# Kernel optimization log

Hardware: AMD Instinct MI355X
Metric: run time of the kernel (lower is better)

## Reference

```python
import jax, jax.numpy as jnp
import numpy as np

EMBED = 1024
HEADS = 16
HEAD_DIM = EMBED // HEADS


def setup_inputs() -> dict:
    key = jax.random.key(0)
    k_x, k_q, k_k, k_v, k_o, k_b = jax.random.split(key, 6)
    s = 1.0 / np.sqrt(EMBED)
    return {
        "x": jax.random.normal(k_x, (4, 2048, EMBED), dtype=jnp.float32),
        "Wq": jax.random.uniform(k_q, (EMBED, EMBED), jnp.float32, -s, s),
        "Wk": jax.random.uniform(k_k, (EMBED, EMBED), jnp.float32, -s, s),
        "Wv": jax.random.uniform(k_v, (EMBED, EMBED), jnp.float32, -s, s),
        "Wo": jax.random.uniform(k_o, (EMBED, EMBED), jnp.float32, -s, s),
        "bo": jax.random.uniform(k_b, (EMBED,), jnp.float32, -s, s),
    }


def reference(x, Wq, Wk, Wv, Wo, bo):
    B, S, E = x.shape
    H, D = HEADS, HEAD_DIM
    # torch nn.Linear: y = x @ W.T
    q = (x @ Wq.T).reshape(B, S, H, D).transpose(0, 2, 1, 3)  # [B,H,S,D]
    k = (x @ Wk.T).reshape(B, S, H, D).transpose(0, 2, 1, 3)
    v = (x @ Wv.T).reshape(B, S, H, D).transpose(0, 2, 1, 3)
    # NOTE: module scales by sqrt(embed_size), not sqrt(head_dim)
    scores = jnp.einsum("bhqd,bhkd->bhqk", q, k) / jnp.sqrt(jnp.float32(E))
    causal = jnp.triu(jnp.ones((S, S), dtype=bool), k=1)
    scores = jnp.where(causal, -jnp.inf, scores)
    attn = jax.nn.softmax(scores, axis=-1)
    out = jnp.einsum("bhqk,bhkd->bhqd", attn, v)  # [B,H,S,D]
    out = out.transpose(0, 2, 1, 3).reshape(B, S, E)
    return out @ Wo.T + bo
```

## Files before the change

kernel.cpp:

```cpp
#include <hip/hip_runtime.h>


#define E_DIM 1024
#define S_LEN 2048
#define BATCH 4
#define NHEAD 16
#define HDIM  64

using short8 = __attribute__((ext_vector_type(8))) short;
using f32x4  = __attribute__((ext_vector_type(4))) float;
using f32x16 = __attribute__((ext_vector_type(16))) float;
using i32x4  = __attribute__((ext_vector_type(4))) int;
using u32x2  = __attribute__((ext_vector_type(2))) unsigned int;

#define GLD16(gp, lp) __builtin_amdgcn_global_load_lds( \
    (const __attribute__((address_space(1))) void*)(gp), \
    (__attribute__((address_space(3))) void*)(lp), 16, 0, 0)

__device__ inline unsigned short f2bf(float f) {
    unsigned int u = __builtin_bit_cast(unsigned int, f);
    u += 0x7FFFu + ((u >> 16) & 1u);
    return (unsigned short)(u >> 16);
}

__device__ inline unsigned int cvt_pk_bf16(float a, float b) {
    unsigned int r;
    asm("v_cvt_pk_bf16_f32 %0, %1, %2" : "=v"(r) : "v"(a), "v"(b));
    return r;
}

__global__ __launch_bounds__(256) void cvt_all(
        const float* __restrict__ x,  const float* __restrict__ wq,
        const float* __restrict__ wk, const float* __restrict__ wv,
        const float* __restrict__ wo,
        unsigned short* __restrict__ xb, unsigned short* __restrict__ wb) {
    const int bid = blockIdx.x;
    const float* src;
    unsigned short* dst;
    int blk;
    if (bid < 8192) { src = x; dst = xb; blk = bid; }
    else {
        const int wsel = (bid - 8192) >> 10;
        blk = (bid - 8192) & 1023;
        src = (wsel == 0) ? wq : (wsel == 1) ? wk : (wsel == 2) ? wv : wo;
        dst = wb + (size_t)wsel * 1048576;
    }
    const int i = (blk * 256 + threadIdx.x) * 4;
    float4 v = *reinterpret_cast<const float4*>(src + i);
    ushort4 o;
    o.x = f2bf(v.x); o.y = f2bf(v.y); o.z = f2bf(v.z); o.w = f2bf(v.w);
    *reinterpret_cast<ushort4*>(dst + i) = o;
}

__global__ __launch_bounds__(256) void gemm_qkv(
        const unsigned short* __restrict__ xb,
        const unsigned short* __restrict__ wb,
        unsigned short* __restrict__ qkv) {
    const int z = blockIdx.z;
    const unsigned short* Bw = wb + (size_t)z * (E_DIM * E_DIM);
    unsigned short* Out = qkv + (size_t)z * ((size_t)BATCH * NHEAD * S_LEN * HDIM);
    const int m0 = blockIdx.x * 128, n0 = blockIdx.y * 128;
    const int tid = threadIdx.x;
    const int lane = tid & 63, w = tid >> 6;
    const int wm = w >> 1, wn = w & 1;
    const int col = lane & 15, hi = lane >> 4;

    __shared__ __align__(16) unsigned short Alds[128 * 32];
    __shared__ __align__(16) unsigned short Blds[128 * 32];

    const int srow = tid >> 2;
    const int sc8  = (tid & 3) * 8;
    const int wofs = w * 512;

    f32x4 acc[4][4] = {};

    for (int kt = 0; kt < E_DIM / 32; ++kt) {
        const int k0 = kt * 32;
        GLD16(xb + (size_t)(m0 + srow) * E_DIM + k0 + sc8,       &Alds[wofs]);
        GLD16(xb + (size_t)(m0 + 64 + srow) * E_DIM + k0 + sc8,  &Alds[2048 + wofs]);
        GLD16(Bw + (size_t)(n0 + srow) * E_DIM + k0 + sc8,       &Blds[wofs]);
        GLD16(Bw + (size_t)(n0 + 64 + srow) * E_DIM + k0 + sc8,  &Blds[2048 + wofs]);
        __syncthreads();
        short8 af[4], bf[4];
#pragma unroll
        for (int mt = 0; mt < 4; ++mt)
            af[mt] = *reinterpret_cast<const short8*>(&Alds[(wm * 64 + mt * 16 + col) * 32 + hi * 8]);
#pragma unroll
        for (int nt = 0; nt < 4; ++nt)
            bf[nt] = *reinterpret_cast<const short8*>(&Blds[(wn * 64 + nt * 16 + col) * 32 + hi * 8]);
#pragma unroll
        for (int mt = 0; mt < 4; ++mt)
#pragma unroll
            for (int nt = 0; nt < 4; ++nt)
                acc[mt][nt] = __builtin_amdgcn_mfma_f32_16x16x32_bf16(af[mt], bf[nt], acc[mt][nt], 0, 0, 0);
        __syncthreads();
    }

    const float scale = (z == 0) ? (0.03125f * 1.44269504f) : 1.0f;
#pragma unroll
    for (int mt = 0; mt < 4; ++mt) {
#pragma unroll
        for (int nt = 0; nt < 4; ++nt) {
#pragma unroll
            for (int b = 0; b < 4; ++b) {
                int m = m0 + wm * 64 + mt * 16 + hi * 4 + b;
                int n = n0 + wn * 64 + nt * 16 + col;
                int bidx = m >> 11, s = m & 2047;
                int h = n >> 6, d = n & 63;
                size_t off = (((size_t)(bidx * NHEAD + h)) * S_LEN + s) * HDIM + d;
                Out[off] = f2bf(acc[mt][nt][b] * scale);
            }
        }
    }
}

__global__ __launch_bounds__(512, 2) void attn_fwd(
        const unsigned short* __restrict__ Q,
        const unsigned short* __restrict__ K,
        const unsigned short* __restrict__ V,
        unsigned short* __restrict__ Out) {
    const int g = blockIdx.x;
    const int qt = 7 - (g >> 6);
    const int bh = (g & 7) + ((g >> 3) & 7) * 8;
    const int b_idx = bh >> 4, h = bh & 15;
    const int tid = threadIdx.x, lane = tid & 63, w = tid >> 6;
    const int l31 = lane & 31, b5 = lane >> 5;
    const int rsw = (l31 & 7) << 3;

    const unsigned short* Qb = Q + (size_t)bh * (S_LEN * HDIM);
    const unsigned short* Kb = K + (size_t)bh * (S_LEN * HDIM);
    const unsigned short* Vb = V + (size_t)bh * (S_LEN * HDIM);

    __shared__ __align__(16) unsigned short Klds[256 * 64];
    __shared__ __align__(16) unsigned short Vt[64 * 256];

    const int krl  = lane >> 3;
    const int kcsw = ((lane & 7) * 8) ^ (krl << 3);
    const int vr = tid & 63, vc8 = (tid >> 6) * 8;

    const int nt = qt + 1;
    const int q0w = qt * 256 + w * 32;
    const int qg = q0w + l31;

    short8 qf[4];
    {
        const unsigned short* qrow = Qb + (size_t)qg * HDIM;
#pragma unroll
        for (int dc = 0; dc < 4; ++dc)
            qf[dc] = *reinterpret_cast<const short8*>(qrow + dc * 16 + b5 * 8);
    }

    f32x16 ot0 = {}, ot1 = {};
    float mrun = -INFINITY, lsum = 0.f;

    short8 pv0 = *reinterpret_cast<const short8*>(Vb + (size_t)(vr) * HDIM + vc8);
    short8 pv1 = *reinterpret_cast<const short8*>(Vb + (size_t)(64 + vr) * HDIM + vc8);
    short8 pv2 = *reinterpret_cast<const short8*>(Vb + (size_t)(128 + vr) * HDIM + vc8);
    short8 pv3 = *reinterpret_cast<const short8*>(Vb + (size_t)(192 + vr) * HDIM + vc8);

    for (int t = 0; t < nt; ++t) {
        const int kv0 = t * 256;
        __syncthreads();
#pragma unroll
        for (int i = 0; i < 4; ++i) {
            const int rowbase = 8 * (8 * i + w);
            GLD16(Kb + (size_t)(kv0 + rowbase + krl) * HDIM + kcsw,
                  &Klds[rowbase * 64]);
        }
#pragma unroll
        for (int j = 0; j < 8; ++j) {
            const int d0 = vc8 + j;
            const int sj = (d0 & 7) << 3;
            Vt[d0 * 256 + ((vr)       ^ sj)] = (unsigned short)pv0[j];
            Vt[d0 * 256 + ((64 + vr)  ^ sj)] = (unsigned short)pv1[j];
            Vt[d0 * 256 + ((128 + vr) ^ sj)] = (unsigned short)pv2[j];
            Vt[d0 * 256 + ((192 + vr) ^ sj)] = (unsigned short)pv3[j];
        }
        if (t < nt - 1) {
            const int kn = kv0 + 256;
            pv0 = *reinterpret_cast<const short8*>(Vb + (size_t)(kn + vr) * HDIM + vc8);
            pv1 = *reinterpret_cast<const short8*>(Vb + (size_t)(kn + 64 + vr) * HDIM + vc8);
            pv2 = *reinterpret_cast<const short8*>(Vb + (size_t)(kn + 128 + vr) * HDIM + vc8);
            pv3 = *reinterpret_cast<const short8*>(Vb + (size_t)(kn + 192 + vr) * HDIM + vc8);
        }
        __syncthreads();

#pragma unroll
        for (int s4 = 0; s4 < 4; ++s4) {
            const int kvs = kv0 + 64 * s4;
            if (kvs > q0w + 31) break;
            const int ksb = 64 * s4;

            f32x16 st0 = {}, st1 = {};
            __builtin_amdgcn_s_setprio(1);
#pragma unroll
            for (int dc = 0; dc < 4; ++dc) {
                const int co = dc * 16 + b5 * 8;
                short8 kfA = *reinterpret_cast<const short8*>(&Klds[(ksb + l31) * 64 + (co ^ rsw)]);
                short8 kfB = *reinterpret_cast<const short8*>(&Klds[(ksb + 32 + l31) * 64 + (co ^ rsw)]);
                st0 = __builtin_amdgcn_mfma_f32_32x32x16_bf16(kfA, qf[dc], st0, 0, 0, 0);
                st1 = __builtin_amdgcn_mfma_f32_32x32x16_bf16(kfB, qf[dc], st1, 0, 0, 0);
            }
            __builtin_amdgcn_s_setprio(0);

            if (kvs + 63 > q0w) {
#pragma unroll
                for (int r = 0; r < 16; ++r) {
                    const int krow = (r & 3) + 8 * (r >> 2) + 4 * b5;
                    if (kvs + krow > qg)      st0[r] = -INFINITY;
                    if (kvs + 32 + krow > qg) st1[r] = -INFINITY;
                }
            }

            float tm0 = fmaxf(st0[0], st1[0]), tm1 = fmaxf(st0[1], st1[1]);
            float tm2 = fmaxf(st0[2], st1[2]), tm3 = fmaxf(st0[3], st1[3]);
            float tm4 = fmaxf(st0[4], st1[4]), tm5 = fmaxf(st0[5], st1[5]);
            float tm6 = fmaxf(st0[6], st1[6]), tm7 = fmaxf(st0[7], st1[7]);
            tm0 = fmaxf(tm0, fmaxf(st0[8],  st1[8]));
            tm1 = fmaxf(tm1, fmaxf(st0[9],  st1[9]));
            tm2 = fmaxf(tm2, fmaxf(st0[10], st1[10]));
            tm3 = fmaxf(tm3, fmaxf(st0[11], st1[11]));
            tm4 = fmaxf(tm4, fmaxf(st0[12], st1[12]));
            tm5 = fmaxf(tm5, fmaxf(st0[13], st1[13]));
            tm6 = fmaxf(tm6, fmaxf(st0[14], st1[14]));
            tm7 = fmaxf(tm7, fmaxf(st0[15], st1[15]));
            tm0 = fmaxf(tm0, tm4); tm1 = fmaxf(tm1, tm5);
            tm2 = fmaxf(tm2, tm6); tm3 = fmaxf(tm3, tm7);
            float vm = fmaxf(fmaxf(tm0, tm1), fmaxf(tm2, tm3));
            vm = fmaxf(vm, __shfl_xor(vm, 32));
            if (__any(vm > mrun + 11.5f)) {
                const float mnew = fmaxf(mrun, vm);
                const float fac = exp2f(mrun - mnew);
                mrun = mnew;
                lsum *= fac;
#pragma unroll
                for (int r = 0; r < 16; ++r) { ot0[r] *= fac; ot1[r] *= fac; }
            }

#pragma unroll
            for (int kc = 0; kc < 4; ++kc) {
                const int r0 = (kc & 1) * 8;
                float pe[8];
#pragma unroll
                for (int i = 0; i < 8; ++i) {
                    const float sv = (kc < 2) ? st0[r0 + i] : st1[r0 + i];
                    pe[i] = exp2f(sv - mrun);
                }
                const float ps = ((pe[0] + pe[1]) + (pe[2] + pe[3]))
                               + ((pe[4] + pe[5]) + (pe[6] + pe[7]));
                lsum += ps;
                const unsigned int W0 = cvt_pk_bf16(pe[0], pe[1]);
                const unsigned int W1 = cvt_pk_bf16(pe[2], pe[3]);
                const unsigned int W2 = cvt_pk_bf16(pe[4], pe[5]);
                const unsigned int W3 = cvt_pk_bf16(pe[6], pe[7]);
                u32x2 s02 = __builtin_amdgcn_permlane32_swap(W0, W2, false, false);
                u32x2 s13 = __builtin_amdgcn_permlane32_swap(W1, W3, false, false);
                i32x4 wv;
                wv[0] = (int)s02[0];
                wv[1] = (int)s13[0];
                wv[2] = (int)s02[1];
                wv[3] = (int)s13[1];
                const short8 pf = __builtin_bit_cast(short8, wv);

                const int ck = ksb + kc * 16 + b5 * 8;
                short8 vf0 = *reinterpret_cast<const short8*>(&Vt[l31 * 256 + (ck ^ rsw)]);
                short8 vf1 = *reinterpret_cast<const short8*>(&Vt[(32 + l31) * 256 + (ck ^ rsw)]);
                __builtin_amdgcn_s_setprio(1);
                ot0 = __builtin_amdgcn_mfma_f32_32x32x16_bf16(vf0, pf, ot0, 0, 0, 0);
                ot1 = __builtin_amdgcn_mfma_f32_32x32x16_bf16(vf1, pf, ot1, 0, 0, 0);
                __builtin_amdgcn_s_setprio(0);
            }
        }
    }

    const float lfull = lsum + __shfl_xor(lsum, 32);
    const float inv = 1.0f / lfull;
    const size_t base = ((size_t)(b_idx * S_LEN + qg)) * E_DIM + h * HDIM;
#pragma unroll
    for (int r2 = 0; r2 < 8; ++r2) {
        const int d0 = 2 * (r2 & 1) + 8 * (r2 >> 1) + 4 * b5;
        const unsigned int u0 = cvt_pk_bf16(ot0[2 * r2] * inv, ot0[2 * r2 + 1] * inv);
        const unsigned int u1 = cvt_pk_bf16(ot1[2 * r2] * inv, ot1[2 * r2 + 1] * inv);
        *reinterpret_cast<unsigned int*>(const_cast<unsigned short*>(Out) + base + d0) = u0;
        *reinterpret_cast<unsigned int*>(const_cast<unsigned short*>(Out) + base + 32 + d0) = u1;
    }
}

__global__ __launch_bounds__(256) void gemm_out(
        const unsigned short* __restrict__ Ab,
        const unsigned short* __restrict__ Bw,
        const float* __restrict__ bias,
        float* __restrict__ Out) {
    const int m0 = blockIdx.x * 128, n0 = blockIdx.y * 128;
    const int tid = threadIdx.x;
    const int lane = tid & 63, w = tid >> 6;
    const int wm = w >> 1, wn = w & 1;
    const int col = lane & 15, hi = lane >> 4;

    __shared__ __align__(16) unsigned short Alds[128 * 32];
    __shared__ __align__(16) unsigned short Blds[128 * 32];

    const int srow = tid >> 2;
    const int sc8  = (tid & 3) * 8;
    const int wofs = w * 512;

    f32x4 acc[4][4] = {};

    for (int kt = 0; kt < E_DIM / 32; ++kt) {
        const int k0 = kt * 32;
        GLD16(Ab + (size_t)(m0 + srow) * E_DIM + k0 + sc8,       &Alds[wofs]);
        GLD16(Ab + (size_t)(m0 + 64 + srow) * E_DIM + k0 + sc8,  &Alds[2048 + wofs]);
        GLD16(Bw + (size_t)(n0 + srow) * E_DIM + k0 + sc8,       &Blds[wofs]);
        GLD16(Bw + (size_t)(n0 + 64 + srow) * E_DIM + k0 + sc8,  &Blds[2048 + wofs]);
        __syncthreads();
        short8 af[4], bf[4];
#pragma unroll
        for (int mt = 0; mt < 4; ++mt)
            af[mt] = *reinterpret_cast<const short8*>(&Alds[(wm * 64 + mt * 16 + col) * 32 + hi * 8]);
#pragma unroll
        for (int nt = 0; nt < 4; ++nt)
            bf[nt] = *reinterpret_cast<const short8*>(&Blds[(wn * 64 + nt * 16 + col) * 32 + hi * 8]);
#pragma unroll
        for (int mt = 0; mt < 4; ++mt)
#pragma unroll
            for (int nt = 0; nt < 4; ++nt)
                acc[mt][nt] = __builtin_amdgcn_mfma_f32_16x16x32_bf16(af[mt], bf[nt], acc[mt][nt], 0, 0, 0);
        __syncthreads();
    }

#pragma unroll
    for (int mt = 0; mt < 4; ++mt) {
#pragma unroll
        for (int nt = 0; nt < 4; ++nt) {
#pragma unroll
            for (int b = 0; b < 4; ++b) {
                int m = m0 + wm * 64 + mt * 16 + hi * 4 + b;
                int n = n0 + wn * 64 + nt * 16 + col;
                Out[(size_t)m * E_DIM + n] = acc[mt][nt][b] + bias[n];
            }
        }
    }
}

extern "C" void kernel_launch(void* const* d_in, const int* in_sizes, int n_in,
                              void* d_out, int out_size, void* d_ws, size_t ws_size,
                              hipStream_t stream) {
    const float* x  = (const float*)d_in[0];
    const float* Wq = (const float*)d_in[1];
    const float* Wk = (const float*)d_in[2];
    const float* Wv = (const float*)d_in[3];
    const float* Wo = (const float*)d_in[4];
    const float* bo = (const float*)d_in[5];
    float* out = (float*)d_out;

    unsigned short* ws   = (unsigned short*)d_ws;
    unsigned short* xb   = ws;
    unsigned short* wb   = xb + (size_t)8192 * 1024;
    unsigned short* qkv  = wb + (size_t)4 * 1024 * 1024;
    unsigned short* attn = qkv + (size_t)3 * 8192 * 1024;

    cvt_all<<<12288, 256, 0, stream>>>(x, Wq, Wk, Wv, Wo, xb, wb);
    gemm_qkv<<<dim3(64, 8, 3), 256, 0, stream>>>(xb, wb, qkv);
    attn_fwd<<<512, 512, 0, stream>>>(qkv, qkv + 8388608, qkv + 2 * 8388608, attn);
    gemm_out<<<dim3(64, 8), 256, 0, stream>>>(attn, wb + 3 * 1048576, bo, out);
}
```

Baseline: 177.2 us.

## Pair causal query tiles per block and double-buffer K/V in LDS

Each attention block now handles two query tiles (qt = 7-p and p), so every block does the same total number of KV tiles and the causal load is balanced. The grid shrinks from 512 to 256 blocks. K and V tiles are double-buffered in LDS, so the next tile's async K load and V transpose-store overlap compute on the current tile, and one barrier per tile replaces two. LDS use doubles to 128 KB per block, which likely drops occupancy from 2 blocks per CU to 1. With 256 blocks that is about one block per CU.

```diff
diff --git a/kernel.cpp b/kernel.cpp
--- a/kernel.cpp
+++ b/kernel.cpp
@@ -120,8 +120,8 @@
         const unsigned short* __restrict__ V,
         unsigned short* __restrict__ Out) {
     const int g = blockIdx.x;
-    const int qt = 7 - (g >> 6);
-    const int bh = (g & 7) + ((g >> 3) & 7) * 8;
+    const int p = g >> 6;
+    const int bh = g & 63;
     const int b_idx = bh >> 4, h = bh & 15;
     const int tid = threadIdx.x, lane = tid & 63, w = tid >> 6;
     const int l31 = lane & 31, b5 = lane >> 5;
@@ -131,158 +131,194 @@
     const unsigned short* Kb = K + (size_t)bh * (S_LEN * HDIM);
     const unsigned short* Vb = V + (size_t)bh * (S_LEN * HDIM);
 
-    __shared__ __align__(16) unsigned short Klds[256 * 64];
-    __shared__ __align__(16) unsigned short Vt[64 * 256];
+    __shared__ __align__(16) unsigned short Klds[2][256 * 64];
+    __shared__ __align__(16) unsigned short Vt[2][64 * 256];
 
     const int krl  = lane >> 3;
     const int kcsw = ((lane & 7) * 8) ^ (krl << 3);
     const int vr = tid & 63, vc8 = (tid >> 6) * 8;
 
-    const int nt = qt + 1;
-    const int q0w = qt * 256 + w * 32;
-    const int qg = q0w + l31;
-
-    short8 qf[4];
-    {
-        const unsigned short* qrow = Qb + (size_t)qg * HDIM;
-#pragma unroll
-        for (int dc = 0; dc < 4; ++dc)
-            qf[dc] = *reinterpret_cast<const short8*>(qrow + dc * 16 + b5 * 8);
-    }
-
-    f32x16 ot0 = {}, ot1 = {};
-    float mrun = -INFINITY, lsum = 0.f;
-
-    short8 pv0 = *reinterpret_cast<const short8*>(Vb + (size_t)(vr) * HDIM + vc8);
-    short8 pv1 = *reinterpret_cast<const short8*>(Vb + (size_t)(64 + vr) * HDIM + vc8);
-    short8 pv2 = *reinterpret_cast<const short8*>(Vb + (size_t)(128 + vr) * HDIM + vc8);
-    short8 pv3 = *reinterpret_cast<const short8*>(Vb + (size_t)(192 + vr) * HDIM + vc8);
-
-    for (int t = 0; t < nt; ++t) {
-        const int kv0 = t * 256;
-        __syncthreads();
+    const int qts[2] = {7 - p, p};
+
+#pragma unroll
+    for (int it = 0; it < 2; ++it) {
+        const int qt = qts[it];
+        const int nt = qt + 1;
+        const int q0w = qt * 256 + w * 32;
+        const int qg = q0w + l31;
+
+        short8 qf[4];
+        {
+            const unsigned short* qrow = Qb + (size_t)qg * HDIM;
+#pragma unroll
+            for (int dc = 0; dc < 4; ++dc)
+                qf[dc] = *reinterpret_cast<const short8*>(qrow + dc * 16 + b5 * 8);
+        }
+
+        f32x16 ot0 = {}, ot1 = {};
+        float mrun = -INFINITY, lsum = 0.f;
+
+        __syncthreads();
+
 #pragma unroll
         for (int i = 0; i < 4; ++i) {
             const int rowbase = 8 * (8 * i + w);
-            GLD16(Kb + (size_t)(kv0 + rowbase + krl) * HDIM + kcsw,
-                  &Klds[rowbase * 64]);
-        }
+            GLD16(Kb + (size_t)(rowbase + krl) * HDIM + kcsw, &Klds[0][rowbase * 64]);
+        }
+        short8 pv0 = *reinterpret_cast<const short8*>(Vb + (size_t)(vr) * HDIM + vc8);
+        short8 pv1 = *reinterpret_cast<const short8*>(Vb + (size_t)(64 + vr) * HDIM + vc8);
+        short8 pv2 = *reinterpret_cast<const short8*>(Vb + (size_t)(128 + vr) * HDIM + vc8);
+        short8 pv3 = *reinterpret_cast<const short8*>(Vb + (size_t)(192 + vr) * HDIM + vc8);
 #pragma unroll
         for (int j = 0; j < 8; ++j) {
             const int d0 = vc8 + j;
             const int sj = (d0 & 7) << 3;
-            Vt[d0 * 256 + ((vr)       ^ sj)] = (unsigned short)pv0[j];
-            Vt[d0 * 256 + ((64 + vr)  ^ sj)] = (unsigned short)pv1[j];
-            Vt[d0 * 256 + ((128 + vr) ^ sj)] = (unsigned short)pv2[j];
-            Vt[d0 * 256 + ((192 + vr) ^ sj)] = (unsigned short)pv3[j];
-        }
-        if (t < nt - 1) {
-            const int kn = kv0 + 256;
-            pv0 = *reinterpret_cast<const short8*>(Vb + (size_t)(kn + vr) * HDIM + vc8);
-            pv1 = *reinterpret_cast<const short8*>(Vb + (size_t)(kn + 64 + vr) * HDIM + vc8);
-            pv2 = *reinterpret_cast<const short8*>(Vb + (size_t)(kn + 128 + vr) * HDIM + vc8);
-            pv3 = *reinterpret_cast<const short8*>(Vb + (size_t)(kn + 192 + vr) * HDIM + vc8);
-        }
-        __syncthreads();
-
-#pragma unroll
-        for (int s4 = 0; s4 < 4; ++s4) {
-            const int kvs = kv0 + 64 * s4;
-            if (kvs > q0w + 31) break;
-            const int ksb = 64 * s4;
-
-            f32x16 st0 = {}, st1 = {};
-            __builtin_amdgcn_s_setprio(1);
-#pragma unroll
-            for (int dc = 0; dc < 4; ++dc) {
-                const int co = dc * 16 + b5 * 8;
-                short8 kfA = *reinterpret_cast<const short8*>(&Klds[(ksb + l31) * 64 + (co ^ rsw)]);
-                short8 kfB = *reinterpret_cast<const short8*>(&Klds[(ksb + 32 + l31) * 64 + (co ^ rsw)]);
-                st0 = __builtin_amdgcn_mfma_f32_32x32x16_bf16(kfA, qf[dc], st0, 0, 0, 0);
-                st1 = __builtin_amdgcn_mfma_f32_32x32x16_bf16(kfB, qf[dc], st1, 0, 0, 0);
+            Vt[0][d0 * 256 + ((vr)       ^ sj)] = (unsigned short)pv0[j];
+            Vt[0][d0 * 256 + ((64 + vr)  ^ sj)] = (unsigned short)pv1[j];
+            Vt[0][d0 * 256 + ((128 + vr) ^ sj)] = (unsigned short)pv2[j];
+            Vt[0][d0 * 256 + ((192 + vr) ^ sj)] = (unsigned short)pv3[j];
+        }
+        if (nt > 1) {
+            pv0 = *reinterpret_cast<const short8*>(Vb + (size_t)(256 + vr) * HDIM + vc8);
+            pv1 = *reinterpret_cast<const short8*>(Vb + (size_t)(256 + 64 + vr) * HDIM + vc8);
+            pv2 = *reinterpret_cast<const short8*>(Vb + (size_t)(256 + 128 + vr) * HDIM + vc8);
+            pv3 = *reinterpret_cast<const short8*>(Vb + (size_t)(256 + 192 + vr) * HDIM + vc8);
+        }
+        __syncthreads();
+
+        int cur = 0;
+        for (int t = 0; t < nt; ++t) {
+            const int kv0 = t * 256;
+            const int nxt = cur ^ 1;
+            if (t + 1 < nt) {
+                const int kn = kv0 + 256;
+#pragma unroll
+                for (int i = 0; i < 4; ++i) {
+                    const int rowbase = 8 * (8 * i + w);
+                    GLD16(Kb + (size_t)(kn + rowbase + krl) * HDIM + kcsw,
+                          &Klds[nxt][rowbase * 64]);
+                }
+#pragma unroll
+                for (int j = 0; j < 8; ++j) {
+                    const int d0 = vc8 + j;
+                    const int sj = (d0 & 7) << 3;
+                    Vt[nxt][d0 * 256 + ((vr)       ^ sj)] = (unsigned short)pv0[j];
+                    Vt[nxt][d0 * 256 + ((64 + vr)  ^ sj)] = (unsigned short)pv1[j];
+                    Vt[nxt][d0 * 256 + ((128 + vr) ^ sj)] = (unsigned short)pv2[j];
+                    Vt[nxt][d0 * 256 + ((192 + vr) ^ sj)] = (unsigned short)pv3[j];
+                }
+                if (t + 2 < nt) {
+                    const int kn2 = kv0 + 512;
+                    pv0 = *reinterpret_cast<const short8*>(Vb + (size_t)(kn2 + vr) * HDIM + vc8);
+                    pv1 = *reinterpret_cast<const short8*>(Vb + (size_t)(kn2 + 64 + vr) * HDIM + vc8);
+                    pv2 = *reinterpret_cast<const short8*>(Vb + (size_t)(kn2 + 128 + vr) * HDIM + vc8);
+                    pv3 = *reinterpret_cast<const short8*>(Vb + (size_t)(kn2 + 192 + vr) * HDIM + vc8);
+                }
             }
-            __builtin_amdgcn_s_setprio(0);
-
-            if (kvs + 63 > q0w) {
-#pragma unroll
-                for (int r = 0; r < 16; ++r) {
-                    const int krow = (r & 3) + 8 * (r >> 2) + 4 * b5;
-                    if (kvs + krow > qg)      st0[r] = -INFINITY;
-                    if (kvs + 32 + krow > qg) st1[r] = -INFINITY;
+
+            const unsigned short* Kc = &Klds[cur][0];
+            const unsigned short* Vc = &Vt[cur][0];
+#pragma unroll
+            for (int s4 = 0; s4 < 4; ++s4) {
+                const int kvs = kv0 + 64 * s4;
+                if (kvs > q0w + 31) break;
+                const int ksb = 64 * s4;
+
+                f32x16 st0 = {}, st1 = {};
+                __builtin_amdgcn_s_setprio(1);
+#pragma unroll
+                for (int dc = 0; dc < 4; ++dc) {
+                    const int co = dc * 16 + b5 * 8;
+                    short8 kfA = *reinterpret_cast<const short8*>(&Kc[(ksb + l31) * 64 + (co ^ rsw)]);
+                    short8 kfB = *reinterpret_cast<const short8*>(&Kc[(ksb + 32 + l31) * 64 + (co ^ rsw)]);
+                    st0 = __builtin_amdgcn_mfma_f32_32x32x16_bf16(kfA, qf[dc], st0, 0, 0, 0);
+                    st1 = __builtin_amdgcn_mfma_f32_32x32x16_bf16(kfB, qf[dc], st1, 0, 0, 0);
+                }
+                __builtin_amdgcn_s_setprio(0);
+
+                if (kvs + 63 > q0w) {
+#pragma unroll
+                    for (int r = 0; r < 16; ++r) {
+                        const int krow = (r & 3) + 8 * (r >> 2) + 4 * b5;
+                        if (kvs + krow > qg)      st0[r] = -INFINITY;
+                        if (kvs + 32 + krow > qg) st1[r] = -INFINITY;
+                    }
+                }
+
+                float tm0 = fmaxf(st0[0], st1[0]), tm1 = fmaxf(st0[1], st1[1]);
+                float tm2 = fmaxf(st0[2], st1[2]), tm3 = fmaxf(st0[3], st1[3]);
+                float tm4 = fmaxf(st0[4], st1[4]), tm5 = fmaxf(st0[5], st1[5]);
+                float tm6 = fmaxf(st0[6], st1[6]), tm7 = fmaxf(st0[7], st1[7]);
+                tm0 = fmaxf(tm0, fmaxf(st0[8],  st1[8]));
+                tm1 = fmaxf(tm1, fmaxf(st0[9],  st1[9]));
+                tm2 = fmaxf(tm2, fmaxf(st0[10], st1[10]));
+                tm3 = fmaxf(tm3, fmaxf(st0[11], st1[11]));
+                tm4 = fmaxf(tm4, fmaxf(st0[12], st1[12]));
+                tm5 = fmaxf(tm5, fmaxf(st0[13], st1[13]));
+                tm6 = fmaxf(tm6, fmaxf(st0[14], st1[14]));
+                tm7 = fmaxf(tm7, fmaxf(st0[15], st1[15]));
+                tm0 = fmaxf(tm0, tm4); tm1 = fmaxf(tm1, tm5);
+                tm2 = fmaxf(tm2, tm6); tm3 = fmaxf(tm3, tm7);
+                float vm = fmaxf(fmaxf(tm0, tm1), fmaxf(tm2, tm3));
+                vm = fmaxf(vm, __shfl_xor(vm, 32));
+                if (__any(vm > mrun + 11.5f)) {
+                    const float mnew = fmaxf(mrun, vm);
+                    const float fac = exp2f(mrun - mnew);
+                    mrun = mnew;
+                    lsum *= fac;
+#pragma unroll
+                    for (int r = 0; r < 16; ++r) { ot0[r] *= fac; ot1[r] *= fac; }
+                }
+
+#pragma unroll
+                for (int kc = 0; kc < 4; ++kc) {
+                    const int r0 = (kc & 1) * 8;
+                    float pe[8];
+#pragma unroll
+                    for (int i = 0; i < 8; ++i) {
+                        const float sv = (kc < 2) ? st0[r0 + i] : st1[r0 + i];
+                        pe[i] = exp2f(sv - mrun);
+                    }
+                    const float ps = ((pe[0] + pe[1]) + (pe[2] + pe[3]))
+                                   + ((pe[4] + pe[5]) + (pe[6] + pe[7]));
+                    lsum += ps;
+                    const unsigned int W0 = cvt_pk_bf16(pe[0], pe[1]);
+                    const unsigned int W1 = cvt_pk_bf16(pe[2], pe[3]);
+                    const unsigned int W2 = cvt_pk_bf16(pe[4], pe[5]);
+                    const unsigned int W3 = cvt_pk_bf16(pe[6], pe[7]);
+                    u32x2 s02 = __builtin_amdgcn_permlane32_swap(W0, W2, false, false);
+                    u32x2 s13 = __builtin_amdgcn_permlane32_swap(W1, W3, false, false);
+                    i32x4 wv;
+                    wv[0] = (int)s02[0];
+                    wv[1] = (int)s13[0];
+                    wv[2] = (int)s02[1];
+                    wv[3] = (int)s13[1];
+                    const short8 pf = __builtin_bit_cast(short8, wv);
+
+                    const int ck = ksb + kc * 16 + b5 * 8;
+                    short8 vf0 = *reinterpret_cast<const short8*>(&Vc[l31 * 256 + (ck ^ rsw)]);
+                    short8 vf1 = *reinterpret_cast<const short8*>(&Vc[(32 + l31) * 256 + (ck ^ rsw)]);
+                    __builtin_amdgcn_s_setprio(1);
+                    ot0 = __builtin_amdgcn_mfma_f32_32x32x16_bf16(vf0, pf, ot0, 0, 0, 0);
+                    ot1 = __builtin_amdgcn_mfma_f32_32x32x16_bf16(vf1, pf, ot1, 0, 0, 0);
+                    __builtin_amdgcn_s_setprio(0);
                 }
             }
-
-            float tm0 = fmaxf(st0[0], st1[0]), tm1 = fmaxf(st0[1], st1[1]);
-            float tm2 = fmaxf(st0[2], st1[2]), tm3 = fmaxf(st0[3], st1[3]);
-            float tm4 = fmaxf(st0[4], st1[4]), tm5 = fmaxf(st0[5], st1[5]);
-            float tm6 = fmaxf(st0[6], st1[6]), tm7 = fmaxf(st0[7], st1[7]);
-            tm0 = fmaxf(tm0, fmaxf(st0[8],  st1[8]));
-            tm1 = fmaxf(tm1, fmaxf(st0[9],  st1[9]));
-            tm2 = fmaxf(tm2, fmaxf(st0[10], st1[10]));
-            tm3 = fmaxf(tm3, fmaxf(st0[11], st1[11]));
-            tm4 = fmaxf(tm4, fmaxf(st0[12], st1[12]));
-            tm5 = fmaxf(tm5, fmaxf(st0[13], st1[13]));
-            tm6 = fmaxf(tm6, fmaxf(st0[14], st1[14]));
-            tm7 = fmaxf(tm7, fmaxf(st0[15], st1[15]));
-            tm0 = fmaxf(tm0, tm4); tm1 = fmaxf(tm1, tm5);
-            tm2 = fmaxf(tm2, tm6); tm3 = fmaxf(tm3, tm7);
-            float vm = fmaxf(fmaxf(tm0, tm1), fmaxf(tm2, tm3));
-            vm = fmaxf(vm, __shfl_xor(vm, 32));
-            if (__any(vm > mrun + 11.5f)) {
-                const float mnew = fmaxf(mrun, vm);
-                const float fac = exp2f(mrun - mnew);
-                mrun = mnew;
-                lsum *= fac;
-#pragma unroll
-                for (int r = 0; r < 16; ++r) { ot0[r] *= fac; ot1[r] *= fac; }
-            }
-
-#pragma unroll
-            for (int kc = 0; kc < 4; ++kc) {
-                const int r0 = (kc & 1) * 8;
-                float pe[8];
-#pragma unroll
-                for (int i = 0; i < 8; ++i) {
-                    const float sv = (kc < 2) ? st0[r0 + i] : st1[r0 + i];
-                    pe[i] = exp2f(sv - mrun);
-                }
-                const float ps = ((pe[0] + pe[1]) + (pe[2] + pe[3]))
-                               + ((pe[4] + pe[5]) + (pe[6] + pe[7]));
-                lsum += ps;
-                const unsigned int W0 = cvt_pk_bf16(pe[0], pe[1]);
-                const unsigned int W1 = cvt_pk_bf16(pe[2], pe[3]);
-                const unsigned int W2 = cvt_pk_bf16(pe[4], pe[5]);
-                const unsigned int W3 = cvt_pk_bf16(pe[6], pe[7]);
-                u32x2 s02 = __builtin_amdgcn_permlane32_swap(W0, W2, false, false);
-                u32x2 s13 = __builtin_amdgcn_permlane32_swap(W1, W3, false, false);
-                i32x4 wv;
-                wv[0] = (int)s02[0];
-                wv[1] = (int)s13[0];
-                wv[2] = (int)s02[1];
-                wv[3] = (int)s13[1];
-                const short8 pf = __builtin_bit_cast(short8, wv);
-
-                const int ck = ksb + kc * 16 + b5 * 8;
-                short8 vf0 = *reinterpret_cast<const short8*>(&Vt[l31 * 256 + (ck ^ rsw)]);
-                short8 vf1 = *reinterpret_cast<const short8*>(&Vt[(32 + l31) * 256 + (ck ^ rsw)]);
-                __builtin_amdgcn_s_setprio(1);
-                ot0 = __builtin_amdgcn_mfma_f32_32x32x16_bf16(vf0, pf, ot0, 0, 0, 0);
-                ot1 = __builtin_amdgcn_mfma_f32_32x32x16_bf16(vf1, pf, ot1, 0, 0, 0);
-                __builtin_amdgcn_s_setprio(0);
-            }
-        }
-    }
-
-    const float lfull = lsum + __shfl_xor(lsum, 32);
-    const float inv = 1.0f / lfull;
-    const size_t base = ((size_t)(b_idx * S_LEN + qg)) * E_DIM + h * HDIM;
-#pragma unroll
-    for (int r2 = 0; r2 < 8; ++r2) {
-        const int d0 = 2 * (r2 & 1) + 8 * (r2 >> 1) + 4 * b5;
-        const unsigned int u0 = cvt_pk_bf16(ot0[2 * r2] * inv, ot0[2 * r2 + 1] * inv);
-        const unsigned int u1 = cvt_pk_bf16(ot1[2 * r2] * inv, ot1[2 * r2 + 1] * inv);
-        *reinterpret_cast<unsigned int*>(const_cast<unsigned short*>(Out) + base + d0) = u0;
-        *reinterpret_cast<unsigned int*>(const_cast<unsigned short*>(Out) + base + 32 + d0) = u1;
+            __syncthreads();
+            cur = nxt;
+        }
+
+        const float lfull = lsum + __shfl_xor(lsum, 32);
+        const float inv = 1.0f / lfull;
+        const size_t base = ((size_t)(b_idx * S_LEN + qg)) * E_DIM + h * HDIM;
+#pragma unroll
+        for (int r2 = 0; r2 < 8; ++r2) {
+            const int d0 = 2 * (r2 & 1) + 8 * (r2 >> 1) + 4 * b5;
+            const unsigned int u0 = cvt_pk_bf16(ot0[2 * r2] * inv, ot0[2 * r2 + 1] * inv);
+            const unsigned int u1 = cvt_pk_bf16(ot1[2 * r2] * inv, ot1[2 * r2 + 1] * inv);
+            *reinterpret_cast<unsigned int*>(const_cast<unsigned short*>(Out) + base + d0) = u0;
+            *reinterpret_cast<unsigned int*>(const_cast<unsigned short*>(Out) + base + 32 + d0) = u1;
+        }
     }
 }
 
@@ -361,6 +397,6 @@
 
     cvt_all<<<12288, 256, 0, stream>>>(x, Wq, Wk, Wv, Wo, xb, wb);
     gemm_qkv<<<dim3(64, 8, 3), 256, 0, stream>>>(xb, wb, qkv);
-    attn_fwd<<<512, 512, 0, stream>>>(qkv, qkv + 8388608, qkv + 2 * 8388608, attn);
+    attn_fwd<<<256, 512, 0, stream>>>(qkv, qkv + 8388608, qkv + 2 * 8388608, attn);
     gemm_out<<<dim3(64, 8), 256, 0, stream>>>(attn, wb + 3 * 1048576, bo, out);
 }
```

After: 184.4 us. +4.1%, slower.
